# Optimization experiments

Measured on AMD Instinct MI355X. Metric: run time of the kernel, lower is better.

The kernel has to match this reference:

```python
import jax, jax.numpy as jnp
import numpy as np

N = 100000   # nodes in batched graph
E = 1600000  # edges
B = 2048     # number of user/item pairs (target links)
IN = 4       # one-hot node label dim
H = 32       # latent dim per layer
R = 5        # num relations (rating levels)
NB = 2       # num bases
L = 4        # num conv layers


def setup_inputs() -> dict:
    key = jax.random.key(0)
    ks = jax.random.split(key, 16)
    s = 0.1
    # node labels: first B nodes are users (class 0), next B items (class 1), rest hop labels {2,3}
    cls = jax.random.randint(ks[0], (N,), 2, IN)
    cls = cls.at[:B].set(0).at[B:2 * B].set(1)
    x = jax.nn.one_hot(cls, IN, dtype=jnp.float32)
    src = jax.random.randint(ks[1], (E,), 0, N)
    dst = jax.random.randint(ks[2], (E,), 0, N)
    etype = jax.random.randint(ks[3], (E,), 0, R)
    V0 = jax.random.normal(ks[4], (NB, IN, H), jnp.float32) * s
    comp0 = jax.random.normal(ks[5], (R, NB), jnp.float32) * s
    loop0 = jax.random.normal(ks[6], (IN, H), jnp.float32) * s
    bias0 = jnp.zeros((H,), jnp.float32)
    Vs = jax.random.normal(ks[7], (L - 1, NB, H, H), jnp.float32) * s
    comps = jax.random.normal(ks[8], (L - 1, R, NB), jnp.float32) * s
    loops = jax.random.normal(ks[9], (L - 1, H, H), jnp.float32) * s
    biases = jnp.zeros((L - 1, H), jnp.float32)
    w1 = jax.random.normal(ks[10], (128, 2 * L * H), jnp.float32) * 0.05
    b1 = jnp.zeros((128,), jnp.float32)
    w2 = jax.random.normal(ks[11], (1, 128), jnp.float32) * 0.05
    b2 = jnp.zeros((1,), jnp.float32)
    return {"x": x, "src": src, "dst": dst, "etype": etype,
            "V0": V0, "comp0": comp0, "loop0": loop0, "bias0": bias0,
            "Vs": Vs, "comps": comps, "loops": loops, "biases": biases,
            "w1": w1, "b1": b1, "w2": w2, "b2": b2}


def _rgcn(h, src, dst, etype, V, comp, loopW, bias):
    # basis-decomposed RelGraphConv: W_r = sum_b comp[r,b] * V[b]
    # precompute per-basis transforms at nodes, then combine per edge by relation coeff
    xb = jnp.einsum('ni,bio->nbo', h, V)            # [N, NB, out]
    m = jnp.einsum('eb,ebo->eo', comp[etype], xb[src])  # [E, out]
    agg = jax.ops.segment_sum(m, dst, num_segments=h.shape[0])  # sum aggregation
    return agg + h @ loopW + bias                   # self-loop + bias


def reference(x, src, dst, etype, V0, comp0, loop0, bias0, Vs, comps, loops, biases, w1, b1, w2, b2):
    states = []
    h = jnp.tanh(_rgcn(x, src, dst, etype, V0, comp0, loop0, bias0))
    states.append(h)
    for i in range(L - 1):
        h = jnp.tanh(_rgcn(h, src, dst, etype, Vs[i], comps[i], loops[i], biases[i]))
        states.append(h)
    cs = jnp.concatenate(states, axis=1)            # [N, L*H]
    # users are nodes [0,B), items are nodes [B,2B) by construction (x[:,0]==1 / x[:,1]==1)
    feat = jnp.concatenate([cs[:B], cs[B:2 * B]], axis=1)  # [B, 2*L*H]
    hid = jax.nn.relu(feat @ w1.T + b1)             # dropout inactive (eval)
    out = (hid @ w2.T + b2)[:, 0] * 1               # multiply_by = 1
    return out
```

## Files before the change

### kernel.cpp

```cpp
#include <hip/hip_runtime.h>
#include <hip/hip_fp16.h>

constexpr int N_  = 100000;
constexpr int E_  = 1600000;
constexpr int B_  = 2048;
constexpr int NT_ = 2 * B_;

constexpr int NPB_SHIFT = 8;
constexpr int NPB = 1 << NPB_SHIFT;
constexpr int KB_ = (N_ + NPB - 1) / NPB;
constexpr int CAP_ = 4608;
constexpr int PCHUNK = 6250;
constexpr int NPBLK = (E_ + PCHUNK - 1) / PCHUNK;
constexpr int NTB_ = NT_ / NPB;
constexpr int HSTR = 21;

__global__ __launch_bounds__(256) void init_kernel(
    const float* __restrict__ x, const float* __restrict__ w1,
    unsigned char* __restrict__ cls, int* __restrict__ flag,
    int* __restrict__ cnt, int* __restrict__ bcur, float* __restrict__ w1t)
{
    const int b = blockIdx.x, t = threadIdx.x;
    if (b < 391) {
        const int n = b * 256 + t;
        if (n < N_) {
            const float4 v = *(const float4*)(x + n * 4);
            cls[n] = v.y > 0.5f ? 1 : (v.z > 0.5f ? 2 : (v.w > 0.5f ? 3 : 0));
            flag[n] = 0;
        }
        if (b == 0 && t == 0) *cnt = 0;
    } else if (b < 519) {
        const int idx = (b - 391) * 256 + t;
        const int j = idx >> 8, k = idx & 255;
        w1t[k * 128 + j] = w1[idx];
    } else {
        for (int i = t; i < KB_; i += 256) bcur[i] = 0;
    }
}

__global__ __launch_bounds__(256) void partition_kernel(
    const int* __restrict__ src, const int* __restrict__ dst,
    const int* __restrict__ etype, int* __restrict__ bcur, int* __restrict__ ebuf)
{
    __shared__ int hist[KB_];
    __shared__ int gbase[KB_];
    __shared__ int lcur[KB_];
    const int t = threadIdx.x;
    for (int i = t; i < KB_; i += 256) { hist[i] = 0; lcur[i] = 0; }
    __syncthreads();
    const int e0 = blockIdx.x * PCHUNK;
    const int e1 = min(e0 + PCHUNK, E_);
    for (int i = e0 + t; i < e1; i += 256) atomicAdd(&hist[dst[i] >> NPB_SHIFT], 1);
    __syncthreads();
    for (int i = t; i < KB_; i += 256) if (hist[i]) gbase[i] = atomicAdd(&bcur[i], hist[i]);
    __syncthreads();
    for (int i = e0 + t; i < e1; i += 256) {
        const int d = dst[i];
        const int b = d >> NPB_SHIFT;
        const int lp = atomicAdd(&lcur[b], 1);
        ebuf[(size_t)b * CAP_ + gbase[b] + lp] = src[i] | (etype[i] << 17) | ((d & (NPB - 1)) << 20);
    }
}

__global__ __launch_bounds__(512) void bfinish_kernel(
    const int* __restrict__ bcur, const int* __restrict__ ebuf,
    const unsigned char* __restrict__ cls,
    const float* __restrict__ comp0, const float* __restrict__ V0,
    const float* __restrict__ loop0, const float* __restrict__ bias0,
    int* __restrict__ rowptr, int* __restrict__ pack,
    float* __restrict__ cs, __half* __restrict__ hout,
    int* __restrict__ flag, int* __restrict__ cnt_g, int* __restrict__ nlist)
{
    __shared__ int cnt[NPB];
    __shared__ int sh[512];
    __shared__ unsigned int hist[NPB * HSTR];
    __shared__ float sLoop[128], sV0[256], sBias[32], sCmp[10];
    __shared__ int lcnt, gbase_s;
    const int b = blockIdx.x, t = threadIdx.x;
    if (b >= KB_) {
        const int tb = b - KB_;
        const int s0 = tb * CAP_;
        const int s1 = s0 + bcur[tb];
        const int nbase = tb << NPB_SHIFT;
        int* lbuf = (int*)hist;
        if (t == 0) lcnt = NPB;
        if (t < NPB) lbuf[t] = nbase + t;
        __syncthreads();
        for (int i = s0 + t; i < s1; i += 512) {
            const int s = ebuf[i] & 0x1FFFF;
            if (s >= NT_ && atomicExch(&flag[s], 1) == 0)
                lbuf[atomicAdd(&lcnt, 1)] = s;
        }
        __syncthreads();
        if (t == 0) gbase_s = atomicAdd(cnt_g, lcnt);
        __syncthreads();
        for (int j = t; j < lcnt; j += 512) nlist[gbase_s + j] = lbuf[j];
        return;
    }
    for (int i = t; i < NPB * HSTR; i += 512) hist[i] = 0u;
    if (t < 128) sLoop[t] = loop0[t];
    if (t < 256) sV0[t]   = V0[t];
    if (t < 32)  sBias[t] = bias0[t];
    if (t < 10)  sCmp[t]  = comp0[t];
    sh[t] = (t < KB_) ? bcur[t] : 0;
    __syncthreads();
#pragma unroll
    for (int off = 1; off < 512; off <<= 1) {
        const int u = (t >= off) ? sh[t - off] : 0;
        __syncthreads();
        sh[t] += u;
        __syncthreads();
    }
    const int myCnt = bcur[b];
    const int db = sh[b] - myCnt;
    const int s0 = b * CAP_;
    const int s1 = s0 + myCnt;
    __syncthreads();
    for (int i = s0 + t; i < s1; i += 512) {
        const int p = ebuf[i];
        const int et_c = ((p >> 17) & 7) * 4 + cls[p & 0x1FFFF];
        atomicAdd(&hist[(p >> 20) * HSTR + et_c], 1u);
    }
    __syncthreads();
    int v = 0;
    if (t < NPB) {
#pragma unroll
        for (int j = 0; j < 20; ++j) v += (int)hist[t * HSTR + j];
    }
    sh[t] = (t < NPB) ? v : 0;
    __syncthreads();
#pragma unroll
    for (int off = 1; off < NPB; off <<= 1) {
        const int u = (t >= off) ? sh[t - off] : 0;
        __syncthreads();
        sh[t] += u;
        __syncthreads();
    }
    const int node = (b << NPB_SHIFT) + t;
    if (t < NPB) {
        const int rp = db + sh[t] - v;
        if (node < N_) rowptr[node] = rp;
        cnt[t] = rp;
    }
    if (b == 0 && t == 0) rowptr[N_] = E_;
    __syncthreads();
    for (int i = s0 + t; i < s1; i += 512) {
        const int p = ebuf[i];
        const int pos = atomicAdd(&cnt[p >> 20], 1);
        pack[pos] = p & 0xFFFFF;
    }
    if (t < NPB && node < N_) {
        float A0[4], A1[4];
#pragma unroll
        for (int j = 0; j < 4; ++j) {
            float a0 = 0.f, a1 = 0.f;
#pragma unroll
            for (int r = 0; r < 5; ++r) {
                const float c = (float)hist[t * HSTR + r * 4 + j];
                a0 += c * sCmp[r * 2];
                a1 += c * sCmp[r * 2 + 1];
            }
            A0[j] = a0; A1[j] = a1;
        }
        const int myc = cls[node];
        __half hrow[32];
        const bool wcs = node < NT_;
#pragma unroll 8
        for (int d = 0; d < 32; ++d) {
            float o = sBias[d] + sLoop[myc * 32 + d];
#pragma unroll
            for (int j = 0; j < 4; ++j)
                o += A0[j] * sV0[j * 32 + d] + A1[j] * sV0[128 + j * 32 + d];
            const float r = tanhf(o);
            hrow[d] = __float2half(r);
            if (wcs) cs[node * 128 + d] = r;
        }
        uint4* dst4 = (uint4*)(hout + (size_t)node * 32);
        const uint4* src4 = (const uint4*)hrow;
        dst4[0] = src4[0]; dst4[1] = src4[1]; dst4[2] = src4[2]; dst4[3] = src4[3];
    }
}

__device__ __forceinline__ void acc_chunk(
    const uint4& v, int pq, bool ok, const __half2* __restrict__ cmp2,
    __half2* h0, __half2* h1)
{
    const int tt = (pq >> 17) & 7;
    const __half2 z = __float2half2_rn(0.f);
    const __half2 c0 = ok ? cmp2[tt * 2]     : z;
    const __half2 c1 = ok ? cmp2[tt * 2 + 1] : z;
    const __half2* hp = (const __half2*)&v;
#pragma unroll
    for (int k = 0; k < 4; ++k) {
        h0[k] = __hfma2(c0, hp[k], h0[k]);
        h1[k] = __hfma2(c1, hp[k], h1[k]);
    }
}

__device__ __forceinline__ float gather_body(
    int n, int lane, int g,
    const __half* __restrict__ hin, const int* __restrict__ rowptr,
    const int* __restrict__ pack, const __half2* __restrict__ cmp2,
    const float* __restrict__ V, const float* __restrict__ loopW,
    const float* __restrict__ bias, float (*hs)[96])
{
    hs[g][lane] = __half2float(hin[n * 32 + lane]);
    const int beg = rowptr[n], end = rowptr[n + 1];
    const int sg = lane >> 2;
    const int c  = lane & 3;
    const int i0 = beg + sg, i1 = i0 + 8, i2 = i0 + 16, i3 = i0 + 24;
    const int p0 = pack[i0 < end ? i0 : beg];
    const int p1 = pack[i1 < end ? i1 : beg];
    const int p2 = pack[i2 < end ? i2 : beg];
    const int p3 = pack[i3 < end ? i3 : beg];
    const uint4 v0 = *(const uint4*)(hin + (size_t)(p0 & 0x1FFFF) * 32 + c * 8);
    const uint4 v1 = *(const uint4*)(hin + (size_t)(p1 & 0x1FFFF) * 32 + c * 8);
    const uint4 v2 = *(const uint4*)(hin + (size_t)(p2 & 0x1FFFF) * 32 + c * 8);
    const uint4 v3 = *(const uint4*)(hin + (size_t)(p3 & 0x1FFFF) * 32 + c * 8);
    __half2 h0[4], h1[4];
    const __half2 z = __float2half2_rn(0.f);
#pragma unroll
    for (int k = 0; k < 4; ++k) { h0[k] = z; h1[k] = z; }
    acc_chunk(v0, p0, i0 < end, cmp2, h0, h1);
    acc_chunk(v1, p1, i1 < end, cmp2, h0, h1);
    acc_chunk(v2, p2, i2 < end, cmp2, h0, h1);
    acc_chunk(v3, p3, i3 < end, cmp2, h0, h1);
    for (int e0 = beg + 32; e0 < end; e0 += 8) {
        const int e = e0 + sg;
        const bool ok = e < end;
        const int p = pack[ok ? e : beg];
        const uint4 u = *(const uint4*)(hin + (size_t)(p & 0x1FFFF) * 32 + c * 8);
        acc_chunk(u, p, ok, cmp2, h0, h1);
    }
#pragma unroll
    for (int m = 4; m <= 16; m <<= 1) {
#pragma unroll
        for (int k = 0; k < 4; ++k) {
            const int r0 = __shfl_xor(__builtin_bit_cast(int, h0[k]), m, 32);
            const int r1 = __shfl_xor(__builtin_bit_cast(int, h1[k]), m, 32);
            h0[k] = __hadd2(h0[k], __builtin_bit_cast(__half2, r0));
            h1[k] = __hadd2(h1[k], __builtin_bit_cast(__half2, r1));
        }
    }
    if (lane < 4) {
#pragma unroll
        for (int k = 0; k < 4; ++k) {
            const float2 f0 = __half22float2(h0[k]);
            const float2 f1 = __half22float2(h1[k]);
            hs[g][32 + c * 8 + 2 * k]     = f0.x;
            hs[g][32 + c * 8 + 2 * k + 1] = f0.y;
            hs[g][64 + c * 8 + 2 * k]     = f1.x;
            hs[g][64 + c * 8 + 2 * k + 1] = f1.y;
        }
    }
    __builtin_amdgcn_wave_barrier();
    float o = bias[lane];
#pragma unroll
    for (int k0 = 0; k0 < 32; k0 += 4) {
        const float4 s  = *(const float4*)&hs[g][k0];
        const float4 sa = *(const float4*)&hs[g][32 + k0];
        const float4 sb = *(const float4*)&hs[g][64 + k0];
        o += s.x  * loopW[(k0 + 0) * 32 + lane] + s.y  * loopW[(k0 + 1) * 32 + lane]
           + s.z  * loopW[(k0 + 2) * 32 + lane] + s.w  * loopW[(k0 + 3) * 32 + lane]
           + sa.x * V[(k0 + 0) * 32 + lane]     + sa.y * V[(k0 + 1) * 32 + lane]
           + sa.z * V[(k0 + 2) * 32 + lane]     + sa.w * V[(k0 + 3) * 32 + lane]
           + sb.x * V[1024 + (k0 + 0) * 32 + lane] + sb.y * V[1024 + (k0 + 1) * 32 + lane]
           + sb.z * V[1024 + (k0 + 2) * 32 + lane] + sb.w * V[1024 + (k0 + 3) * 32 + lane];
    }
    return tanhf(o);
}

__global__ __launch_bounds__(256) void gather_kernel(
    const __half* __restrict__ hin, const int* __restrict__ rowptr,
    const int* __restrict__ pack, const float* __restrict__ comp,
    const float* __restrict__ V, const float* __restrict__ loopW,
    const float* __restrict__ bias,
    float* __restrict__ cs, __half* __restrict__ hout, int out_off)
{
    __shared__ __align__(16) float hs[8][96];
    __shared__ __half2 cmp2[10];
    const int t = threadIdx.x, lane = t & 31, g = t >> 5;
    if (lane < 10) cmp2[lane] = __float2half2_rn(comp[lane]);
    __builtin_amdgcn_wave_barrier();
    const int n = blockIdx.x * 8 + g;
    const float r = gather_body(n, lane, g, hin, rowptr, pack, cmp2, V, loopW, bias, hs);
    if (n < NT_) cs[n * 128 + out_off + lane] = r;
    hout[n * 32 + lane] = __float2half(r);
}

__global__ __launch_bounds__(256) void gatherL_kernel(
    const __half* __restrict__ hin, const int* __restrict__ rowptr,
    const int* __restrict__ pack, const float* __restrict__ comp,
    const float* __restrict__ V, const float* __restrict__ loopW,
    const float* __restrict__ bias,
    const int* __restrict__ nlist, const int* __restrict__ cnt,
    float* __restrict__ cs, __half* __restrict__ hout, int out_off)
{
    __shared__ __align__(16) float hs[8][96];
    __shared__ __half2 cmp2[10];
    const int t = threadIdx.x, lane = t & 31, g = t >> 5;
    if (lane < 10) cmp2[lane] = __float2half2_rn(comp[lane]);
    __builtin_amdgcn_wave_barrier();
    const int idx = blockIdx.x * 8 + g;
    if (idx >= *cnt) return;
    const int n = nlist[idx];
    const float r = gather_body(n, lane, g, hin, rowptr, pack, cmp2, V, loopW, bias, hs);
    if (n < NT_) cs[n * 128 + out_off + lane] = r;
    hout[n * 32 + lane] = __float2half(r);
}

__global__ __launch_bounds__(128) void mlp_kernel(
    const __half* __restrict__ hin, const int* __restrict__ rowptr,
    const int* __restrict__ pack, const float* __restrict__ comp,
    const float* __restrict__ V, const float* __restrict__ loopW,
    const float* __restrict__ bias,
    const float* __restrict__ cs, const float* __restrict__ w1t,
    const float* __restrict__ b1, const float* __restrict__ w2,
    const float* __restrict__ b2, float* __restrict__ out)
{
    __shared__ __align__(16) float feat[256];
    __shared__ __align__(16) float hs[2][96];
    __shared__ __half2 cmp2[10];
    __shared__ float part[2];
    const int p = blockIdx.x, t = threadIdx.x;
    if (t < 10) cmp2[t] = __float2half2_rn(comp[t]);
    if (t < 64) {
        const int g = t >> 5, lane = t & 31;
        const int n = g ? (B_ + p) : p;
        const float r = gather_body(n, lane, g, hin, rowptr, pack, cmp2, V, loopW, bias, hs);
        feat[g * 128 + 96 + lane] = r;
    } else {
        const int i = t - 64;
        for (int j = i; j < 96; j += 64) {
            feat[j]       = cs[p * 128 + j];
            feat[128 + j] = cs[(B_ + p) * 128 + j];
        }
    }
    __syncthreads();
    float acc = b1[t];
#pragma unroll
    for (int k0 = 0; k0 < 256; k0 += 4) {
        const float4 f = *(const float4*)&feat[k0];
        acc += f.x * w1t[(k0 + 0) * 128 + t] + f.y * w1t[(k0 + 1) * 128 + t]
             + f.z * w1t[(k0 + 2) * 128 + t] + f.w * w1t[(k0 + 3) * 128 + t];
    }
    const float hid = acc > 0.f ? acc : 0.f;
    float v = w2[t] * hid;
#pragma unroll
    for (int off = 32; off > 0; off >>= 1) v += __shfl_down(v, off, 64);
    if ((t & 63) == 0) part[t >> 6] = v;
    __syncthreads();
    if (t == 0) out[p] = part[0] + part[1] + b2[0];
}

extern "C" void kernel_launch(void* const* d_in, const int* in_sizes, int n_in,
                              void* d_out, int out_size, void* d_ws, size_t ws_size,
                              hipStream_t stream) {
    const float* x      = (const float*)d_in[0];
    const int*   src    = (const int*)d_in[1];
    const int*   dst    = (const int*)d_in[2];
    const int*   etype  = (const int*)d_in[3];
    const float* V0     = (const float*)d_in[4];
    const float* comp0  = (const float*)d_in[5];
    const float* loop0  = (const float*)d_in[6];
    const float* bias0  = (const float*)d_in[7];
    const float* Vs     = (const float*)d_in[8];
    const float* comps  = (const float*)d_in[9];
    const float* loops  = (const float*)d_in[10];
    const float* biases = (const float*)d_in[11];
    const float* w1     = (const float*)d_in[12];
    const float* b1     = (const float*)d_in[13];
    const float* w2     = (const float*)d_in[14];
    const float* b2     = (const float*)d_in[15];
    float* out = (float*)d_out;

    float* ws   = (float*)d_ws;
    float* cs   = ws;
    float* w1t  = cs + (size_t)NT_ * 128;
    __half* hA  = (__half*)(w1t + 256 * 128);
    __half* hB  = hA + (size_t)N_ * 32;
    int* ebuf   = (int*)(hB + (size_t)N_ * 32);
    int* pack   = ebuf + (size_t)KB_ * CAP_;
    int* rowptr = pack + E_;
    int* flag   = rowptr + N_ + 1;
    int* cnt    = flag + N_;
    int* nlist  = cnt + 1;
    int* bcur   = nlist + N_;
    unsigned char* cls = (unsigned char*)(bcur + KB_);

    const int gathBlocks = N_ / 8;

    init_kernel<<<520, 256, 0, stream>>>(x, w1, cls, flag, cnt, bcur, w1t);
    partition_kernel<<<NPBLK, 256, 0, stream>>>(src, dst, etype, bcur, ebuf);
    bfinish_kernel<<<KB_ + NTB_, 512, 0, stream>>>(bcur, ebuf, cls, comp0, V0, loop0, bias0,
                                                   rowptr, pack, cs, hA, flag, cnt, nlist);
    gather_kernel<<<gathBlocks, 256, 0, stream>>>(
        hA, rowptr, pack, comps + 0, Vs + 0, loops + 0, biases + 0, cs, hB, 32);
    gatherL_kernel<<<gathBlocks, 256, 0, stream>>>(
        hB, rowptr, pack, comps + 10, Vs + 2048, loops + 1024, biases + 32,
        nlist, cnt, cs, hA, 64);
    mlp_kernel<<<B_, 128, 0, stream>>>(
        hA, rowptr, pack, comps + 20, Vs + 4096, loops + 2048, biases + 64,
        cs, w1t, b1, w2, b2, out);
}
```

Before: 159.3 us.

## Fold init into partition kernel and batch eight pairs per MLP block

The separate init kernel is merged into the partition kernel as extra blocks, and the counter zeroing is replaced with a memset over bcur and an adjacent cnt slot. The final MLP kernel now handles eight user/item pairs per 256-thread block, so each w1t load is reused across four feature rows. The aims are to drop one kernel launch and cut redundant weight traffic in the MLP. The partition blocks read bcur in the same kernel that the extra blocks run in, but bcur is zeroed beforehand by the memset, so ordering holds.

New measurement: 163.5 us. 2.6% more time.

```diff
diff --git a/kernel.cpp b/kernel.cpp
--- a/kernel.cpp
+++ b/kernel.cpp
@@ -14,41 +14,37 @@
 constexpr int NPBLK = (E_ + PCHUNK - 1) / PCHUNK;
 constexpr int NTB_ = NT_ / NPB;
 constexpr int HSTR = 21;
-
-__global__ __launch_bounds__(256) void init_kernel(
+constexpr int PPB = 8;
+
+__global__ __launch_bounds__(256) void partition_kernel(
     const float* __restrict__ x, const float* __restrict__ w1,
-    unsigned char* __restrict__ cls, int* __restrict__ flag,
-    int* __restrict__ cnt, int* __restrict__ bcur, float* __restrict__ w1t)
+    const int* __restrict__ src, const int* __restrict__ dst,
+    const int* __restrict__ etype, int* __restrict__ bcur, int* __restrict__ ebuf,
+    unsigned char* __restrict__ cls, int* __restrict__ flag, float* __restrict__ w1t)
 {
     const int b = blockIdx.x, t = threadIdx.x;
-    if (b < 391) {
-        const int n = b * 256 + t;
-        if (n < N_) {
-            const float4 v = *(const float4*)(x + n * 4);
-            cls[n] = v.y > 0.5f ? 1 : (v.z > 0.5f ? 2 : (v.w > 0.5f ? 3 : 0));
-            flag[n] = 0;
-        }
-        if (b == 0 && t == 0) *cnt = 0;
-    } else if (b < 519) {
-        const int idx = (b - 391) * 256 + t;
-        const int j = idx >> 8, k = idx & 255;
-        w1t[k * 128 + j] = w1[idx];
-    } else {
-        for (int i = t; i < KB_; i += 256) bcur[i] = 0;
-    }
-}
-
-__global__ __launch_bounds__(256) void partition_kernel(
-    const int* __restrict__ src, const int* __restrict__ dst,
-    const int* __restrict__ etype, int* __restrict__ bcur, int* __restrict__ ebuf)
-{
+    if (b >= NPBLK) {
+        const int bb = b - NPBLK;
+        if (bb < 391) {
+            const int n = bb * 256 + t;
+            if (n < N_) {
+                const float4 v = *(const float4*)(x + n * 4);
+                cls[n] = v.y > 0.5f ? 1 : (v.z > 0.5f ? 2 : (v.w > 0.5f ? 3 : 0));
+                flag[n] = 0;
+            }
+        } else {
+            const int idx = (bb - 391) * 256 + t;
+            const int j = idx >> 8, k = idx & 255;
+            w1t[k * 128 + j] = w1[idx];
+        }
+        return;
+    }
     __shared__ int hist[KB_];
     __shared__ int gbase[KB_];
     __shared__ int lcur[KB_];
-    const int t = threadIdx.x;
     for (int i = t; i < KB_; i += 256) { hist[i] = 0; lcur[i] = 0; }
     __syncthreads();
-    const int e0 = blockIdx.x * PCHUNK;
+    const int e0 = b * PCHUNK;
     const int e1 = min(e0 + PCHUNK, E_);
     for (int i = e0 + t; i < e1; i += 256) atomicAdd(&hist[dst[i] >> NPB_SHIFT], 1);
     __syncthreads();
@@ -56,9 +52,9 @@
     __syncthreads();
     for (int i = e0 + t; i < e1; i += 256) {
         const int d = dst[i];
-        const int b = d >> NPB_SHIFT;
-        const int lp = atomicAdd(&lcur[b], 1);
-        ebuf[(size_t)b * CAP_ + gbase[b] + lp] = src[i] | (etype[i] << 17) | ((d & (NPB - 1)) << 20);
+        const int bk = d >> NPB_SHIFT;
+        const int lp = atomicAdd(&lcur[bk], 1);
+        ebuf[(size_t)bk * CAP_ + gbase[bk] + lp] = src[i] | (etype[i] << 17) | ((d & (NPB - 1)) << 20);
     }
 }
 
@@ -309,7 +305,7 @@
     hout[n * 32 + lane] = __float2half(r);
 }
 
-__global__ __launch_bounds__(128) void mlp_kernel(
+__global__ __launch_bounds__(256) void mlp_kernel(
     const __half* __restrict__ hin, const int* __restrict__ rowptr,
     const int* __restrict__ pack, const float* __restrict__ comp,
     const float* __restrict__ V, const float* __restrict__ loopW,
@@ -318,39 +314,55 @@
     const float* __restrict__ b1, const float* __restrict__ w2,
     const float* __restrict__ b2, float* __restrict__ out)
 {
-    __shared__ __align__(16) float feat[256];
-    __shared__ __align__(16) float hs[2][96];
+    __shared__ __align__(16) float feat[PPB][256];
+    __shared__ __align__(16) float hs[8][96];
     __shared__ __half2 cmp2[10];
-    __shared__ float part[2];
-    const int p = blockIdx.x, t = threadIdx.x;
-    if (t < 10) cmp2[t] = __float2half2_rn(comp[t]);
-    if (t < 64) {
-        const int g = t >> 5, lane = t & 31;
-        const int n = g ? (B_ + p) : p;
-        const float r = gather_body(n, lane, g, hin, rowptr, pack, cmp2, V, loopW, bias, hs);
-        feat[g * 128 + 96 + lane] = r;
-    } else {
-        const int i = t - 64;
-        for (int j = i; j < 96; j += 64) {
-            feat[j]       = cs[p * 128 + j];
-            feat[128 + j] = cs[(B_ + p) * 128 + j];
-        }
-    }
-    __syncthreads();
-    float acc = b1[t];
-#pragma unroll
+    __shared__ float red[PPB][2];
+    const int t = threadIdx.x, lane = t & 31, g = t >> 5;
+    const int p0 = blockIdx.x * PPB;
+    if (lane < 10) cmp2[lane] = __float2half2_rn(comp[lane]);
+    __builtin_amdgcn_wave_barrier();
+#pragma unroll
+    for (int r = 0; r < 2; ++r) {
+        const int idx = r * 8 + g;
+        const int pp = idx >> 1, who = idx & 1;
+        const int n = who ? (B_ + p0 + pp) : (p0 + pp);
+        const float rv = gather_body(n, lane, g, hin, rowptr, pack, cmp2, V, loopW, bias, hs);
+        feat[pp][who * 128 + 96 + lane] = rv;
+        const int base = n * 128;
+        feat[pp][who * 128 + lane]      = cs[base + lane];
+        feat[pp][who * 128 + 32 + lane] = cs[base + 32 + lane];
+        feat[pp][who * 128 + 64 + lane] = cs[base + 64 + lane];
+    }
+    __syncthreads();
+    const int j = t & 127;
+    const int half = t >> 7;
+    const int wInHalf = (t >> 6) & 1;
+    const float bj = b1[j], w2j = w2[j];
+    float acc[4];
+#pragma unroll
+    for (int i = 0; i < 4; ++i) acc[i] = bj;
+#pragma unroll 4
     for (int k0 = 0; k0 < 256; k0 += 4) {
-        const float4 f = *(const float4*)&feat[k0];
-        acc += f.x * w1t[(k0 + 0) * 128 + t] + f.y * w1t[(k0 + 1) * 128 + t]
-             + f.z * w1t[(k0 + 2) * 128 + t] + f.w * w1t[(k0 + 3) * 128 + t];
-    }
-    const float hid = acc > 0.f ? acc : 0.f;
-    float v = w2[t] * hid;
-#pragma unroll
-    for (int off = 32; off > 0; off >>= 1) v += __shfl_down(v, off, 64);
-    if ((t & 63) == 0) part[t >> 6] = v;
-    __syncthreads();
-    if (t == 0) out[p] = part[0] + part[1] + b2[0];
+        const float wa = w1t[(k0 + 0) * 128 + j];
+        const float wb = w1t[(k0 + 1) * 128 + j];
+        const float wc = w1t[(k0 + 2) * 128 + j];
+        const float wd = w1t[(k0 + 3) * 128 + j];
+#pragma unroll
+        for (int i = 0; i < 4; ++i) {
+            const float4 f = *(const float4*)&feat[half * 4 + i][k0];
+            acc[i] += f.x * wa + f.y * wb + f.z * wc + f.w * wd;
+        }
+    }
+#pragma unroll
+    for (int i = 0; i < 4; ++i) {
+        float v = w2j * (acc[i] > 0.f ? acc[i] : 0.f);
+#pragma unroll
+        for (int off = 32; off > 0; off >>= 1) v += __shfl_down(v, off, 64);
+        if ((t & 63) == 0) red[half * 4 + i][wInHalf] = v;
+    }
+    __syncthreads();
+    if (t < PPB) out[p0 + t] = red[t][0] + red[t][1] + b2[0];
 }
 
 extern "C" void kernel_launch(void* const* d_in, const int* in_sizes, int n_in,
@@ -383,15 +395,16 @@
     int* pack   = ebuf + (size_t)KB_ * CAP_;
     int* rowptr = pack + E_;
     int* flag   = rowptr + N_ + 1;
-    int* cnt    = flag + N_;
-    int* nlist  = cnt + 1;
+    int* nlist  = flag + N_;
     int* bcur   = nlist + N_;
-    unsigned char* cls = (unsigned char*)(bcur + KB_);
+    int* cnt    = bcur + KB_;
+    unsigned char* cls = (unsigned char*)(cnt + 1);
 
     const int gathBlocks = N_ / 8;
 
-    init_kernel<<<520, 256, 0, stream>>>(x, w1, cls, flag, cnt, bcur, w1t);
-    partition_kernel<<<NPBLK, 256, 0, stream>>>(src, dst, etype, bcur, ebuf);
+    hipMemsetAsync(bcur, 0, (size_t)(KB_ + 1) * sizeof(int), stream);
+    partition_kernel<<<NPBLK + 391 + 128, 256, 0, stream>>>(
+        x, w1, src, dst, etype, bcur, ebuf, cls, flag, w1t);
     bfinish_kernel<<<KB_ + NTB_, 512, 0, stream>>>(bcur, ebuf, cls, comp0, V0, loop0, bias0,
                                                    rowptr, pack, cs, hA, flag, cnt, nlist);
     gather_kernel<<<gathBlocks, 256, 0, stream>>>(
@@ -399,7 +412,7 @@
     gatherL_kernel<<<gathBlocks, 256, 0, stream>>>(
         hB, rowptr, pack, comps + 10, Vs + 2048, loops + 1024, biases + 32,
         nlist, cnt, cs, hA, 64);
-    mlp_kernel<<<B_, 128, 0, stream>>>(
+    mlp_kernel<<<B_ / PPB, 256, 0, stream>>>(
         hA, rowptr, pack, comps + 20, Vs + 4096, loops + 2048, biases + 64,
         cs, w1t, b1, w2, b2, out);
 }
```
